# Kernel tuning notes

Measured on AMD Instinct MI355X. Metric: run time of the kernel, lower is better.

The kernel has to match this reference:

```python
import jax, jax.numpy as jnp
from jax import lax
import numpy as np

NS, NC = 12, 4            # n_state, n_ctrl
NSC = NS + NC             # tau = [x; u]
T, B = 50, 2048
U_LO, U_HI = -1.0, 1.0
LQR_ITERS = 3             # qp_iter-style outer LQR iterations
N_LS = 5                  # max_linesearch_iter
LS_DECAY = 0.5            # linesearch_decay


def setup_inputs() -> dict:
    key = jax.random.key(0)
    k0, k1, k2, k3, k4 = jax.random.split(key, 5)
    x0 = jax.random.normal(k0, (B, NS), jnp.float32)
    # PD quadratic cost: C = 0.1 * A A^T + I  (symmetric positive definite)
    A = jax.random.normal(k1, (T, B, NSC, NSC), jnp.float32) * (1.0 / np.sqrt(NSC))
    C = 0.1 * jnp.einsum('tbik,tbjk->tbij', A, A) + jnp.eye(NSC, dtype=jnp.float32)
    c = jax.random.normal(k2, (T, B, NSC), jnp.float32)
    # Near-identity stable linear dynamics x' = F [x;u] + f
    F = 0.02 * jax.random.normal(k3, (T, B, NS, NSC), jnp.float32)
    eye_pad = jnp.concatenate([0.98 * jnp.eye(NS, dtype=jnp.float32),
                               jnp.zeros((NS, NC), jnp.float32)], axis=-1)
    F = F + eye_pad
    f = 0.01 * jax.random.normal(k4, (T, B, NS), jnp.float32)
    return {'x0': x0, 'C': C, 'c': c, 'F': F, 'f': f}


def _riccati(C, c, F, f):
    """Backward Riccati recursion. Returns feedback gains K [T,B,NC,NS], k [T,B,NC]."""
    def step(carry, inp):
        V, v = carry                      # V: [B,NS,NS], v: [B,NS]
        Ct, ct, Ft, ft = inp
        FtV = jnp.einsum('bki,bkl->bil', Ft, V)          # F^T V: [B,NSC,NS]
        Q = Ct + jnp.einsum('bil,blj->bij', FtV, Ft)     # [B,NSC,NSC]
        q = ct + jnp.einsum('bki,bk->bi', Ft,
                            jnp.einsum('bij,bj->bi', V, ft) + v)
        Qxx, Qxu = Q[:, :NS, :NS], Q[:, :NS, NS:]
        Qux, Quu = Q[:, NS:, :NS], Q[:, NS:, NS:]
        qx, qu = q[:, :NS], q[:, NS:]
        rhs = jnp.concatenate([Qux, qu[:, :, None]], axis=-1)  # [B,NC,NS+1]
        sol = jnp.linalg.solve(Quu, rhs)
        K = -sol[:, :, :NS]               # [B,NC,NS]
        kk = -sol[:, :, NS]               # [B,NC]
        QxuK = jnp.einsum('bij,bjk->bik', Qxu, K)
        V_new = Qxx + QxuK + QxuK.transpose(0, 2, 1) \
            + jnp.einsum('bji,bjl,blk->bik', K, Quu, K)
        V_new = 0.5 * (V_new + V_new.transpose(0, 2, 1))
        v_new = qx + jnp.einsum('bij,bj->bi', Qxu, kk) \
            + jnp.einsum('bji,bj->bi', K, qu + jnp.einsum('bij,bj->bi', Quu, kk))
        return (V_new, v_new), (K, kk)

    Vz = jnp.zeros((C.shape[1], NS, NS), C.dtype)
    vz = jnp.zeros((C.shape[1], NS), C.dtype)
    _, (K, kk) = lax.scan(step, (Vz, vz), (C, c, F, f), reverse=True)
    return K, kk


def _rollout(alpha, x0, u_nom, K, kk, C, c, F, f):
    """Forward pass with box-clamped controls and line-search blending."""
    def step(carry, inp):
        x, cost = carry
        Ct, ct, Ft, ft, Kt, kt, unomt = inp
        u_lqr = jnp.einsum('bij,bj->bi', Kt, x) + kt
        u = jnp.clip((1.0 - alpha) * unomt + alpha * u_lqr, U_LO, U_HI)
        tau = jnp.concatenate([x, u], axis=-1)            # [B,NSC]
        cost = cost + 0.5 * jnp.einsum('bi,bij,bj->b', tau, Ct, tau) \
            + jnp.einsum('bi,bi->b', ct, tau)
        x_next = jnp.einsum('bij,bj->bi', Ft, tau) + ft
        return (x_next, cost), tau

    init = (x0, jnp.zeros(x0.shape[0], x0.dtype))
    (_, cost), taus = lax.scan(step, init, (C, c, F, f, K, kk, u_nom))
    return cost, taus  # cost [B], taus [T,B,NSC]


def reference(x0, C, c, F, f):
    alphas = LS_DECAY ** jnp.arange(N_LS, dtype=C.dtype)  # [N_LS]
    u_nom = jnp.zeros((T, x0.shape[0], NC), x0.dtype)
    taus = None
    for _ in range(LQR_ITERS):
        K, kk = _riccati(C, c, F, f)
        costs, taus_all = jax.vmap(
            lambda a: _rollout(a, x0, u_nom, K, kk, C, c, F, f))(alphas)
        # costs: [N_LS,B]; taus_all: [N_LS,T,B,NSC]. Pick best alpha per batch elem.
        best = jnp.argmin(costs, axis=0)                  # [B]
        taus = jnp.take_along_axis(taus_all,
                                   best[None, None, :, None], axis=0)[0]
        u_nom = taus[:, :, NS:]
    return taus  # [T, B, NSC] optimized trajectory [x; u]
```

## Files before the change

kernel.cpp:

```cpp
#include <hip/hip_runtime.h>
#include <math.h>

#define T_   50
#define B_   2048
#define NS_  12
#define NC_  4
#define NSC_ 16
#define LDC  20
#define AST  808

__device__ __forceinline__ float dot4f(const float4 a, const float4 b) {
    return a.x*b.x + a.y*b.y + a.z*b.z + a.w*b.w;
}
__device__ __forceinline__ void axpy4(float4& acc, float s, const float4 v) {
    acc.x += s*v.x; acc.y += s*v.y; acc.z += s*v.z; acc.w += s*v.w;
}

__device__ __forceinline__ void wsync() {
    __builtin_amdgcn_wave_barrier();
    __builtin_amdgcn_s_waitcnt(0xC07F);
    __builtin_amdgcn_wave_barrier();
}

__device__ __forceinline__ float qsum(float v) {
    v += __int_as_float(__builtin_amdgcn_update_dpp(
            0, __float_as_int(v), 0xB1, 0xF, 0xF, true));
    v += __int_as_float(__builtin_amdgcn_update_dpp(
            0, __float_as_int(v), 0x4E, 0xF, 0xF, true));
    return v;
}

struct RicPref { float4 rC, rAux; };

__device__ __forceinline__ RicPref ric_load(
    const float* Cg, const float* cg, const float* Fg, const float* fg,
    int t, int b, int lane)
{
    RicPref p;
    const size_t base = (size_t)t * B_ + b;
    p.rC = ((const float4*)(Cg + base*256))[lane];
    if (lane < 48)      p.rAux = ((const float4*)(Fg + base*192))[lane];
    else if (lane < 52) p.rAux = ((const float4*)(cg + base*16))[lane-48];
    else if (lane < 55) p.rAux = ((const float4*)(fg + base*12))[lane-52];
    return p;
}

__global__ __launch_bounds__(64) void riccati_kernel(
    const float* __restrict__ Cg, const float* __restrict__ cg,
    const float* __restrict__ Fg, const float* __restrict__ fg,
    float* __restrict__ Kk)
{
    const int b    = blockIdx.x;
    const int lane = threadIdx.x;

    __shared__ __align__(16) float sV[144];
    __shared__ __align__(16) float sv[12];
    __shared__ __align__(16) float sF[12*LDC];
    __shared__ __align__(16) float sFT[16*12];
    __shared__ __align__(16) float sc[16];
    __shared__ __align__(16) float sf[12];
    __shared__ __align__(16) float sP[12*LDC];
    __shared__ __align__(16) float sQ[16*LDC];
    __shared__ __align__(16) float sq[16];
    __shared__ __align__(16) float stmp[12];
    __shared__ __align__(16) float sKT[56];
    __shared__ __align__(16) float sM[144];

    for (int i = lane; i < 144; i += 64) sV[i] = 0.f;
    if (lane < 12) sv[lane] = 0.f;

    RicPref cur = ric_load(Cg, cg, Fg, fg, T_-1, b, lane);
    wsync();

    for (int t = T_ - 1; t >= 0; --t) {
        const size_t base = (size_t)t * B_ + b;

        wsync();
        const float4 rCq = cur.rC;
        {
            const int row = lane >> 2, chx = lane & 3;
            if (lane < 48) {
                *(float4*)(sF + row*LDC + (chx<<2)) = cur.rAux;
                sFT[(4*chx+0)*12 + row] = cur.rAux.x;
                sFT[(4*chx+1)*12 + row] = cur.rAux.y;
                sFT[(4*chx+2)*12 + row] = cur.rAux.z;
                sFT[(4*chx+3)*12 + row] = cur.rAux.w;
            }
            else if (lane < 52) ((float4*)sc)[lane-48] = cur.rAux;
            else if (lane < 55) ((float4*)sf)[lane-52] = cur.rAux;
        }
        RicPref nxt = ric_load(Cg, cg, Fg, fg, (t > 0) ? t-1 : 0, b, lane);
        wsync();

        if (lane < 48) {
            const int k = lane >> 2, jc = (lane & 3) << 2;
            const float4 v0 = *(const float4*)(sV + k*12);
            const float4 v1 = *(const float4*)(sV + k*12 + 4);
            const float4 v2 = *(const float4*)(sV + k*12 + 8);
            const float vk[12] = {v0.x,v0.y,v0.z,v0.w, v1.x,v1.y,v1.z,v1.w,
                                  v2.x,v2.y,v2.z,v2.w};
            float4 acc = make_float4(0.f,0.f,0.f,0.f);
            #pragma unroll
            for (int l = 0; l < 12; ++l)
                axpy4(acc, vk[l], *(const float4*)(sF + l*LDC + jc));
            *(float4*)(sP + k*LDC + jc) = acc;
            if (jc == 0) {
                float accT = sv[k]
                    + dot4f(v0, *(const float4*)(sf))
                    + dot4f(v1, *(const float4*)(sf+4))
                    + dot4f(v2, *(const float4*)(sf+8));
                stmp[k] = accT;
            }
        }
        wsync();

        {
            const int i = lane >> 2, jc = (lane & 3) << 2;
            const float4 f0 = *(const float4*)(sFT + i*12);
            const float4 f1 = *(const float4*)(sFT + i*12 + 4);
            const float4 f2 = *(const float4*)(sFT + i*12 + 8);
            const float fcol[12] = {f0.x,f0.y,f0.z,f0.w, f1.x,f1.y,f1.z,f1.w,
                                    f2.x,f2.y,f2.z,f2.w};
            float4 acc = rCq;
            #pragma unroll
            for (int k = 0; k < 12; ++k)
                axpy4(acc, fcol[k], *(const float4*)(sP + k*LDC + jc));
            *(float4*)(sQ + i*LDC + jc) = acc;
            if (jc == 0) {
                const float accq = sc[i]
                    + dot4f(f0, *(const float4*)(stmp))
                    + dot4f(f1, *(const float4*)(stmp+4))
                    + dot4f(f2, *(const float4*)(stmp+8));
                sq[i] = accq;
                if (i >= 12) sQ[i*LDC + 16] = accq;
            }
        }
        wsync();

        {
            const float4 u0 = *(const float4*)(sQ + 12*LDC + 12);
            const float4 u1 = *(const float4*)(sQ + 13*LDC + 12);
            const float4 u2 = *(const float4*)(sQ + 14*LDC + 12);
            const float4 u3 = *(const float4*)(sQ + 15*LDC + 12);
            const float l00 = sqrtf(u0.x), i00 = 1.f/l00;
            const float l10 = u0.y*i00, l20 = u0.z*i00, l30 = u0.w*i00;
            const float l11 = sqrtf(u1.y - l10*l10), i11 = 1.f/l11;
            const float l21 = (u1.z - l20*l10)*i11;
            const float l31 = (u1.w - l30*l10)*i11;
            const float l22 = sqrtf(u2.z - l20*l20 - l21*l21), i22 = 1.f/l22;
            const float l32 = (u2.w - l30*l20 - l31*l21)*i22;
            const float l33 = sqrtf(u3.w - l30*l30 - l31*l31 - l32*l32), i33 = 1.f/l33;
            if (lane < 13) {
                const int cidx = (lane < 12) ? lane : 16;
                const float r0 = sQ[12*LDC + cidx];
                const float r1 = sQ[13*LDC + cidx];
                const float r2 = sQ[14*LDC + cidx];
                const float r3 = sQ[15*LDC + cidx];
                const float y0 = r0*i00;
                const float y1 = (r1 - l10*y0)*i11;
                const float y2 = (r2 - l20*y0 - l21*y1)*i22;
                const float y3 = (r3 - l30*y0 - l31*y1 - l32*y2)*i33;
                const float z3 = y3*i33;
                const float z2 = (y2 - l32*z3)*i22;
                const float z1 = (y1 - l21*z2 - l31*z3)*i11;
                const float z0 = (y0 - l10*z1 - l20*z2 - l30*z3)*i00;
                *(float4*)(sKT + lane*4) = make_float4(-z0,-z1,-z2,-z3);
            }
        }
        wsync();

        if (lane < 52) {
            float val;
            if (lane < 48) {
                const int i2 = lane / 12, j2 = lane - i2*12;
                val = sKT[j2*4 + i2];
            } else val = sKT[lane];
            (Kk + base*52)[lane] = val;
        }
        if (lane < 36) {
            const int i = lane / 3, jc = (lane % 3) << 2;
            const float4 kv = *(const float4*)(sKT + i*4);
            float4 acc = make_float4(0.f,0.f,0.f,0.f);
            axpy4(acc, kv.x, *(const float4*)(sQ + 12*LDC + jc));
            axpy4(acc, kv.y, *(const float4*)(sQ + 13*LDC + jc));
            axpy4(acc, kv.z, *(const float4*)(sQ + 14*LDC + jc));
            axpy4(acc, kv.w, *(const float4*)(sQ + 15*LDC + jc));
            *(float4*)(sM + i*12 + jc) = acc;
        } else if (lane < 48) {
            const int i = lane - 36;
            const float4 qxu = *(const float4*)(sQ + i*LDC + 12);
            const float4 kk4 = *(const float4*)(sKT + 48);
            sv[i] = sq[i] + dot4f(qxu, kk4);
        }
        wsync();

        if (lane < 36) {
            const int i = lane / 3, jc = (lane % 3) << 2;
            const float4 q  = *(const float4*)(sQ + i*LDC + jc);
            const float4 m1 = *(const float4*)(sM + i*12 + jc);
            const float t0 = sM[(jc+0)*12 + i];
            const float t1 = sM[(jc+1)*12 + i];
            const float t2 = sM[(jc+2)*12 + i];
            const float t3 = sM[(jc+3)*12 + i];
            float4 rr;
            rr.x = q.x + 0.5f*(m1.x + t0);
            rr.y = q.y + 0.5f*(m1.y + t1);
            rr.z = q.z + 0.5f*(m1.z + t2);
            rr.w = q.w + 0.5f*(m1.w + t3);
            *(float4*)(sV + i*12 + jc) = rr;
        }
        cur = nxt;
    }
}

struct RP { float4 C, F, K0, K1, K2; float kk, cr, fr; };

__device__ __forceinline__ RP rp_load(
    const float* __restrict__ Cg, const float* __restrict__ cg,
    const float* __restrict__ Fg, const float* __restrict__ fg,
    const float* __restrict__ Kg, int t, int b, int lane, int r)
{
    RP p;
    const size_t base = (size_t)t * B_ + b;
    p.C  = ((const float4*)(Cg + base*256))[lane];
    p.cr = cg[base*16 + r];
    if (lane < 48) {
        p.F  = ((const float4*)(Fg + base*192))[lane];
        p.fr = fg[base*12 + r];
    }
    if (lane < 20) {
        const float* Kr = Kg + base*52 + (lane & 3)*12;
        p.K0 = *(const float4*)(Kr);
        p.K1 = *(const float4*)(Kr + 4);
        p.K2 = *(const float4*)(Kr + 8);
        p.kk = Kg[base*52 + 48 + (lane & 3)];
    }
    return p;
}

__global__ __launch_bounds__(64) void rollout_kernel(
    const float* __restrict__ x0g, const float* __restrict__ Cg,
    const float* __restrict__ cg,  const float* __restrict__ Fg,
    const float* __restrict__ fg,  const float* __restrict__ Kk,
    float* __restrict__ outg)
{
    const int b    = blockIdx.x;
    const int lane = threadIdx.x;
    const int r  = lane >> 2, ch = lane & 3;
    const bool lo = (lane < 48);
    const float alpha_u = ldexpf(1.f, -r);

    __shared__ __align__(16) float staus[5*AST + 16];
    __shared__ __align__(16) float sunom[T_*NC_];

    float x0v = 0.f;
    if (lo) x0v = x0g[b*12 + r];
    if (lane < 50) *(float4*)(sunom + lane*4) = make_float4(0.f,0.f,0.f,0.f);

    RP cur = rp_load(Cg, cg, Fg, fg, Kk, 0, b, lane, r);
    wsync();

    for (int iter = 0; iter < 3; ++iter) {
        float tau_r[5], cacc[5], xnew[5];
        #pragma unroll
        for (int a = 0; a < 5; ++a) { tau_r[a] = x0v; cacc[a] = 0.f; }
        if (lo) {
            staus[ch*AST + r] = x0v;
            if (ch == 0) staus[4*AST + r] = x0v;
        }

        for (int t = 0; t < T_; ++t) {
            wsync();
            if (lane < 20) {
                const float* xb = staus + r*AST + t*16;
                const float4 xA = *(const float4*)(xb);
                const float4 xB = *(const float4*)(xb + 4);
                const float4 xC = *(const float4*)(xb + 8);
                const float ulqr = dot4f(cur.K0, xA) + dot4f(cur.K1, xB)
                                 + dot4f(cur.K2, xC) + cur.kk;
                float u = (1.f - alpha_u)*sunom[t*4 + ch] + alpha_u*ulqr;
                u = fminf(1.f, fmaxf(-1.f, u));
                staus[r*AST + t*16 + 12 + ch] = u;
            }
            RP nxt = rp_load(Cg, cg, Fg, fg, Kk, (t+1 < T_) ? t+1 : 0, b, lane, r);
            wsync();
            #pragma unroll
            for (int a = 0; a < 5; ++a) {
                const float4 c4 = *(const float4*)(staus + a*AST + t*16 + (ch<<2));
                if (!lo) tau_r[a] = staus[a*AST + t*16 + r];
                float contrib = 0.5f * dot4f(cur.C, c4);
                if (ch == 0) contrib += cur.cr;
                cacc[a] += contrib * tau_r[a];
                if (lo) xnew[a] = qsum(dot4f(cur.F, c4)) + cur.fr;
            }
            if (lo) {
                staus[ch*AST + (t+1)*16 + r] = xnew[ch];
                if (ch == 0) staus[4*AST + (t+1)*16 + r] = xnew[4];
                #pragma unroll
                for (int a = 0; a < 5; ++a) tau_r[a] = xnew[a];
            }
            cur = nxt;
        }

        wsync();
        #pragma unroll
        for (int a = 0; a < 5; ++a) {
            float v = cacc[a];
            #pragma unroll
            for (int off = 1; off < 64; off <<= 1) v += __shfl_xor(v, off, 64);
            cacc[a] = v;
        }
        int best = 0; float bc = cacc[0];
        #pragma unroll
        for (int a = 1; a < 5; ++a)
            if (cacc[a] < bc) { bc = cacc[a]; best = a; }

        if (lane < 50)
            *(float4*)(sunom + lane*4) =
                *(const float4*)(staus + best*AST + lane*16 + 12);
        if (iter == 2 && lane < 50) {
            const float* src = staus + best*AST + lane*16;
            float* dst = outg + ((size_t)lane*B_ + b)*16;
            *(float4*)(dst)      = *(const float4*)(src);
            *(float4*)(dst + 4)  = *(const float4*)(src + 4);
            *(float4*)(dst + 8)  = *(const float4*)(src + 8);
            *(float4*)(dst + 12) = *(const float4*)(src + 12);
        }
    }
}

extern "C" void kernel_launch(void* const* d_in, const int* in_sizes, int n_in,
                              void* d_out, int out_size, void* d_ws, size_t ws_size,
                              hipStream_t stream) {
    const float* x0 = (const float*)d_in[0];
    const float* C  = (const float*)d_in[1];
    const float* c  = (const float*)d_in[2];
    const float* F  = (const float*)d_in[3];
    const float* f  = (const float*)d_in[4];
    float* out = (float*)d_out;
    float* Kk  = (float*)d_ws;

    riccati_kernel<<<B_, 64, 0, stream>>>(C, c, F, f, Kk);
    rollout_kernel<<<B_, 64, 0, stream>>>(x0, C, c, F, f, Kk, out);
}
```

Baseline: 464.9 us.

## Split rollout line-search alphas across five wavefronts per block

The rollout kernel now launches 320 threads per batch element, one wavefront per line-search alpha, in place of a single wavefront that looped over all five alphas. Each wave computes the control from K·x with a DPP quad reduction, using lanes for rows 12-15 of a combined F/K register tile, then computes the next state and the cost. The best alpha is picked through shared memory and block barriers. This shortens the serial per-timestep chain, at the cost of five times the threads and five redundant loads of C/F/K per block.

```diff
diff --git a/kernel.cpp b/kernel.cpp
--- a/kernel.cpp
+++ b/kernel.cpp
@@ -7,7 +7,7 @@
 #define NC_  4
 #define NSC_ 16
 #define LDC  20
-#define AST  808
+#define AST  816
 
 __device__ __forceinline__ float dot4f(const float4 a, const float4 b) {
     return a.x*b.x + a.y*b.y + a.z*b.z + a.w*b.w;
@@ -213,119 +213,105 @@
     }
 }
 
-struct RP { float4 C, F, K0, K1, K2; float kk, cr, fr; };
-
-__device__ __forceinline__ RP rp_load(
+struct RW { float4 C4, G4; float cr, gr; };
+
+__device__ __forceinline__ RW rw_load(
     const float* __restrict__ Cg, const float* __restrict__ cg,
     const float* __restrict__ Fg, const float* __restrict__ fg,
-    const float* __restrict__ Kg, int t, int b, int lane, int r)
+    const float* __restrict__ Kg,
+    int t, int b, int lane, int r, int ch)
 {
-    RP p;
+    RW p;
     const size_t base = (size_t)t * B_ + b;
-    p.C  = ((const float4*)(Cg + base*256))[lane];
+    p.C4 = ((const float4*)(Cg + base*256))[lane];
     p.cr = cg[base*16 + r];
-    if (lane < 48) {
-        p.F  = ((const float4*)(Fg + base*192))[lane];
-        p.fr = fg[base*12 + r];
-    }
-    if (lane < 20) {
-        const float* Kr = Kg + base*52 + (lane & 3)*12;
-        p.K0 = *(const float4*)(Kr);
-        p.K1 = *(const float4*)(Kr + 4);
-        p.K2 = *(const float4*)(Kr + 8);
-        p.kk = Kg[base*52 + 48 + (lane & 3)];
+    if (r < 12) {
+        p.G4 = ((const float4*)(Fg + base*192))[lane];
+        p.gr = fg[base*12 + r];
+    } else {
+        if (ch < 3) p.G4 = *(const float4*)(Kg + base*52 + (r-12)*12 + 4*ch);
+        else        p.G4 = make_float4(0.f,0.f,0.f,0.f);
+        p.gr = Kg[base*52 + 48 + (r-12)];
     }
     return p;
 }
 
-__global__ __launch_bounds__(64) void rollout_kernel(
+__global__ __launch_bounds__(320, 8) void rollout_kernel(
     const float* __restrict__ x0g, const float* __restrict__ Cg,
     const float* __restrict__ cg,  const float* __restrict__ Fg,
     const float* __restrict__ fg,  const float* __restrict__ Kk,
     float* __restrict__ outg)
 {
     const int b    = blockIdx.x;
-    const int lane = threadIdx.x;
-    const int r  = lane >> 2, ch = lane & 3;
-    const bool lo = (lane < 48);
-    const float alpha_u = ldexpf(1.f, -r);
-
-    __shared__ __align__(16) float staus[5*AST + 16];
+    const int tid  = threadIdx.x;
+    const int a    = tid >> 6;
+    const int lane = tid & 63;
+    const int r = lane >> 2, ch = lane & 3;
+    const float alpha = ldexpf(1.f, -a);
+
+    __shared__ __align__(16) float staus[5*AST];
     __shared__ __align__(16) float sunom[T_*NC_];
-
-    float x0v = 0.f;
-    if (lo) x0v = x0g[b*12 + r];
-    if (lane < 50) *(float4*)(sunom + lane*4) = make_float4(0.f,0.f,0.f,0.f);
-
-    RP cur = rp_load(Cg, cg, Fg, fg, Kk, 0, b, lane, r);
-    wsync();
+    __shared__ float scost[5];
+    float* sta = staus + a*AST;
+
+    if (tid < T_*NC_) sunom[tid] = 0.f;
+    if (lane < 12) sta[lane] = x0g[b*12 + lane];
+    RW cur = rw_load(Cg, cg, Fg, fg, Kk, 0, b, lane, r, ch);
+    __syncthreads();
 
     for (int iter = 0; iter < 3; ++iter) {
-        float tau_r[5], cacc[5], xnew[5];
+        float cacc = 0.f;
+
+        for (int t = 0; t < T_; ++t) {
+            float4 c4 = *(const float4*)(sta + t*16 + (ch<<2));
+            const int   ui = (r >= 12) ? (r - 12) : 0;
+            const float un = sunom[t*4 + ui];
+            const float pG1 = (ch < 3) ? dot4f(cur.G4, c4) : 0.f;
+            float       pCt = (ch < 3) ? dot4f(cur.C4, c4) : 0.f;
+            const float q1  = qsum(pG1);
+            if (r >= 12 && ch == 0) {
+                float u = (1.f - alpha)*un + alpha*(q1 + cur.gr);
+                u = fminf(1.f, fmaxf(-1.f, u));
+                sta[t*16 + 12 + (r - 12)] = u;
+            }
+            RW nxt = rw_load(Cg, cg, Fg, fg, Kk,
+                             (t+1 < T_) ? t+1 : 0, b, lane, r, ch);
+            wsync();
+
+            const float4 u4 = *(const float4*)(sta + t*16 + 12);
+            if (ch == 3) { c4 = u4; pCt = dot4f(cur.C4, u4); }
+            const float q2 = qsum((ch == 3) ? dot4f(cur.G4, u4) : 0.f);
+            const float cc = qsum(pCt);
+            if (r < 12 && ch == 0)
+                sta[(t+1)*16 + r] = q1 + q2 + cur.gr;
+            if (ch == (r >> 2)) {
+                const int  sel  = r & 3;
+                const float taur = (sel == 0) ? c4.x : (sel == 1) ? c4.y
+                                  : (sel == 2) ? c4.z : c4.w;
+                cacc += (0.5f*cc + cur.cr) * taur;
+            }
+            cur = nxt;
+            wsync();
+        }
+
+        float v = cacc;
         #pragma unroll
-        for (int a = 0; a < 5; ++a) { tau_r[a] = x0v; cacc[a] = 0.f; }
-        if (lo) {
-            staus[ch*AST + r] = x0v;
-            if (ch == 0) staus[4*AST + r] = x0v;
-        }
-
-        for (int t = 0; t < T_; ++t) {
-            wsync();
-            if (lane < 20) {
-                const float* xb = staus + r*AST + t*16;
-                const float4 xA = *(const float4*)(xb);
-                const float4 xB = *(const float4*)(xb + 4);
-                const float4 xC = *(const float4*)(xb + 8);
-                const float ulqr = dot4f(cur.K0, xA) + dot4f(cur.K1, xB)
-                                 + dot4f(cur.K2, xC) + cur.kk;
-                float u = (1.f - alpha_u)*sunom[t*4 + ch] + alpha_u*ulqr;
-                u = fminf(1.f, fmaxf(-1.f, u));
-                staus[r*AST + t*16 + 12 + ch] = u;
-            }
-            RP nxt = rp_load(Cg, cg, Fg, fg, Kk, (t+1 < T_) ? t+1 : 0, b, lane, r);
-            wsync();
-            #pragma unroll
-            for (int a = 0; a < 5; ++a) {
-                const float4 c4 = *(const float4*)(staus + a*AST + t*16 + (ch<<2));
-                if (!lo) tau_r[a] = staus[a*AST + t*16 + r];
-                float contrib = 0.5f * dot4f(cur.C, c4);
-                if (ch == 0) contrib += cur.cr;
-                cacc[a] += contrib * tau_r[a];
-                if (lo) xnew[a] = qsum(dot4f(cur.F, c4)) + cur.fr;
-            }
-            if (lo) {
-                staus[ch*AST + (t+1)*16 + r] = xnew[ch];
-                if (ch == 0) staus[4*AST + (t+1)*16 + r] = xnew[4];
-                #pragma unroll
-                for (int a = 0; a < 5; ++a) tau_r[a] = xnew[a];
-            }
-            cur = nxt;
-        }
-
-        wsync();
+        for (int off = 1; off < 64; off <<= 1) v += __shfl_xor(v, off, 64);
+        if (lane == 0) scost[a] = v;
+        __syncthreads();
+        int best = 0; float bc = scost[0];
         #pragma unroll
-        for (int a = 0; a < 5; ++a) {
-            float v = cacc[a];
-            #pragma unroll
-            for (int off = 1; off < 64; off <<= 1) v += __shfl_xor(v, off, 64);
-            cacc[a] = v;
-        }
-        int best = 0; float bc = cacc[0];
-        #pragma unroll
-        for (int a = 1; a < 5; ++a)
-            if (cacc[a] < bc) { bc = cacc[a]; best = a; }
-
-        if (lane < 50)
-            *(float4*)(sunom + lane*4) =
-                *(const float4*)(staus + best*AST + lane*16 + 12);
-        if (iter == 2 && lane < 50) {
-            const float* src = staus + best*AST + lane*16;
-            float* dst = outg + ((size_t)lane*B_ + b)*16;
-            *(float4*)(dst)      = *(const float4*)(src);
-            *(float4*)(dst + 4)  = *(const float4*)(src + 4);
-            *(float4*)(dst + 8)  = *(const float4*)(src + 8);
-            *(float4*)(dst + 12) = *(const float4*)(src + 12);
-        }
+        for (int a2 = 1; a2 < 5; ++a2)
+            if (scost[a2] < bc) { bc = scost[a2]; best = a2; }
+
+        if (tid < T_*NC_)
+            sunom[tid] = staus[best*AST + (tid >> 2)*16 + 12 + (tid & 3)];
+        if (iter == 2 && tid < 200) {
+            const int tt = tid >> 2, jo = (tid & 3) << 2;
+            *(float4*)(outg + ((size_t)tt*B_ + b)*16 + jo) =
+                *(const float4*)(staus + best*AST + tt*16 + jo);
+        }
+        __syncthreads();
     }
 }
 
@@ -341,5 +327,5 @@
     float* Kk  = (float*)d_ws;
 
     riccati_kernel<<<B_, 64, 0, stream>>>(C, c, F, f, Kk);
-    rollout_kernel<<<B_, 64, 0, stream>>>(x0, C, c, F, f, Kk, out);
-}
+    rollout_kernel<<<B_, 320, 0, stream>>>(x0, C, c, F, f, Kk, out);
+}
```

Result: slower. 585.8 us (+26.0%).
